# Kernel tuning notes

Hardware: AMD Instinct MI355X
Metric: run time of the kernel (lower is better)

The kernel has to match this reference:

```python
import jax, jax.numpy as jnp
import numpy as np

# channel indices (consistent with INPUT_CHANNELS=6)
WALL, SRC_REAL, SRC_IMAG, GATE_REAL, GATE_IMAG = 0, 1, 2, 3, 4
READOUT_THRESHOLD = 0.35
EPS = 1e-08


def _neighbor_sum(a):
    # zero-padded 4-neighbor shift-sum over last two dims of [B,1,H,W]
    H, W = a.shape[-2], a.shape[-1]
    p = jnp.pad(a, ((0, 0), (0, 0), (1, 1), (1, 1)))
    return (p[:, :, 0:H, 1:W + 1] + p[:, :, 2:H + 2, 1:W + 1]
            + p[:, :, 1:H + 1, 0:W] + p[:, :, 1:H + 1, 2:W + 2])


def _phase_vectors(phase_classes):
    k = jnp.arange(phase_classes, dtype=jnp.float32)
    th = 2.0 * jnp.pi * k / phase_classes
    return jnp.stack([jnp.cos(th), jnp.sin(th)], axis=1)  # [P,2]


def _fixed_logits(vec, phase_classes):
    phases = _phase_vectors(phase_classes)
    mag2 = jnp.sum(vec ** 2, axis=1)
    none = (READOUT_THRESHOLD * READOUT_THRESHOLD - mag2) * 8.0
    phase_logits = (vec @ phases.T - READOUT_THRESHOLD) * 12.0
    return jnp.concatenate([none[:, None], phase_logits], axis=1)


def setup_inputs() -> dict:
    key = jax.random.key(0)
    k1, k2 = jax.random.split(key)
    x = jax.random.uniform(k1, (32, 6, 256, 256), dtype=jnp.float32)
    target = jax.random.randint(k2, (32, 2), 0, 256, dtype=jnp.int64 if jax.config.jax_enable_x64 else jnp.int32)
    return {"x": x, "target": target, "steps": 24}


def reference(x, target, steps):
    phase_classes = 8
    free = 1.0 - x[:, WALL:WALL + 1]
    gate_r = x[:, GATE_REAL:GATE_REAL + 1]
    gate_i = x[:, GATE_IMAG:GATE_IMAG + 1]
    wallf = (x[:, WALL:WALL + 1] > 0.5).astype(x.dtype)

    real = x[:, SRC_REAL:SRC_REAL + 1] * free
    imag = x[:, SRC_IMAG:SRC_IMAG + 1] * free
    written = (real ** 2 + imag ** 2) > EPS
    state_r, state_i = real, imag

    def step(carry, _):
        real, imag, sr, si, written = carry
        inc_r = _neighbor_sum(real)
        inc_i = _neighbor_sum(imag)
        # FIXED_PRISMION: complex multiply with gate
        nr = inc_r * gate_r - inc_i * gate_i
        ni = inc_r * gate_i + inc_i * gate_r
        pre_wall = jnp.mean(jnp.sqrt(nr * nr + ni * ni) * wallf)
        real = nr * free
        imag = ni * free
        active = ((real ** 2 + imag ** 2) > EPS) & (~written)
        sr = jnp.where(active, real, sr)
        si = jnp.where(active, imag, si)
        written = written | active
        real = jnp.where(active, real, jnp.zeros_like(real))
        imag = jnp.where(active, imag, jnp.zeros_like(imag))
        act = jnp.mean(jnp.abs(real) + jnp.abs(imag))
        return (real, imag, sr, si, written), (pre_wall, act)

    (real, imag, state_r, state_i, written), (pre_walls, acts) = jax.lax.scan(
        step, (real, imag, state_r, state_i, written), None, length=int(steps))

    vec_map = jnp.concatenate([state_r, state_i], axis=1)  # [B,2,H,W]
    wall = x[:, WALL:WALL + 1] > 0.5
    leak = jnp.mean((((jnp.sum(vec_map ** 2, axis=1, keepdims=True) ** 0.5) > 0.5) & wall).astype(x.dtype))
    pre_wall_mean = jnp.mean(pre_walls)
    act_mean = jnp.mean(acts)

    b = jnp.arange(vec_map.shape[0])
    vec = vec_map[b, :, target[:, 0], target[:, 1]]  # [B,2]
    logits = _fixed_logits(vec, phase_classes)
    return logits, leak, pre_wall_mean, act_mean
```

## Files before the change

kernel.cpp:

```cpp
#include <hip/hip_runtime.h>
#include <stdint.h>

#define EPSV 1e-8f
#define HH 256
#define WW 256
#define NB 32
#define STEPS 24
#define PLANE (HH * WW)
#define NCELL (NB * PLANE)
#define NBLK 2048
#define TBLK 512
#define CAP 8192
#define FIXS 68719476736.0


__device__ __forceinline__ float block_fsum(float v, float* sm) {
  #pragma unroll
  for (int o = 32; o; o >>= 1) v += __shfl_down(v, o, 64);
  if ((threadIdx.x & 63) == 0) sm[threadIdx.x >> 6] = v;
  __syncthreads();
  float r = 0.0f;
  if (threadIdx.x == 0) r = ((sm[0] + sm[1]) + sm[2]) + sm[3];
  __syncthreads();
  return r;
}

__device__ __forceinline__ int block_isum(int v, int* sm) {
  #pragma unroll
  for (int o = 32; o; o >>= 1) v += __shfl_down(v, o, 64);
  if ((threadIdx.x & 63) == 0) sm[threadIdx.x >> 6] = v;
  __syncthreads();
  int r = 0;
  if (threadIdx.x == 0) r = sm[0] + sm[1] + sm[2] + sm[3];
  __syncthreads();
  return r;
}

__device__ __forceinline__ int block_any(int v, int* sm) {
  if (threadIdx.x == 0) sm[0] = 0;
  __syncthreads();
  if (v) sm[0] = 1;
  __syncthreads();
  int r = sm[0];
  __syncthreads();
  return r;
}

__global__ __launch_bounds__(128) void zero_kernel(int* __restrict__ ctrl) {
  ctrl[threadIdx.x] = 0;
}

__device__ __forceinline__ float2 init_rn(const float* __restrict__ xw, int y, int xc) {
  if ((unsigned)y >= (unsigned)HH || (unsigned)xc >= (unsigned)WW)
    return make_float2(0.f, 0.f);
  const int yx = y * WW + xc;
  const float fr = __fsub_rn(1.0f, xw[yx]);
  return make_float2(__fmul_rn(xw[PLANE + yx], fr), __fmul_rn(xw[2 * PLANE + yx], fr));
}

__device__ __forceinline__ float2 pre0_rn(const float* __restrict__ xw, int y, int xc) {
  float2 up = init_rn(xw, y - 1, xc);
  float2 dn = init_rn(xw, y + 1, xc);
  float2 lf = init_rn(xw, y, xc - 1);
  float2 rg = init_rn(xw, y, xc + 1);
  float inc_r = __fadd_rn(__fadd_rn(__fadd_rn(up.x, dn.x), lf.x), rg.x);
  float inc_i = __fadd_rn(__fadd_rn(__fadd_rn(up.y, dn.y), lf.y), rg.y);
  const int yx = y * WW + xc;
  const float gr = xw[3 * PLANE + yx], gi = xw[4 * PLANE + yx];
  return make_float2(__fsub_rn(__fmul_rn(inc_r, gr), __fmul_rn(inc_i, gi)),
                     __fadd_rn(__fmul_rn(inc_r, gi), __fmul_rn(inc_i, gr)));
}

__device__ __forceinline__ float2 val0_abm(const float* __restrict__ xw,
                                           const uint32_t* __restrict__ abm,
                                           int cbase, int y, int xc) {
  if ((unsigned)y >= (unsigned)HH || (unsigned)xc >= (unsigned)WW)
    return make_float2(0.f, 0.f);
  const int c = cbase + y * WW + xc;
  if (!((abm[c >> 5] >> (c & 31)) & 1u)) return make_float2(0.f, 0.f);
  float2 p = pre0_rn(xw, y, xc);
  const float fr = __fsub_rn(1.0f, xw[y * WW + xc]);
  return make_float2(__fmul_rn(p.x, fr), __fmul_rn(p.y, fr));
}

__global__ __launch_bounds__(256) void fused0_kernel(
    const float* __restrict__ x, const int* __restrict__ target,
    uint32_t* __restrict__ wrw, uint32_t* __restrict__ wrw1,
    uint32_t* __restrict__ abm,
    float* __restrict__ pw_part, float* __restrict__ act_part,
    int* __restrict__ ileak_part, float* __restrict__ vec,
    int* __restrict__ ctrl, int* __restrict__ list, uint32_t* __restrict__ cbm) {
  __shared__ float smf[4];
  __shared__ int smi[4];
  const int tx = threadIdx.x;
  const int blk = blockIdx.x;
  const int b = blk >> 6;
  const int y0 = (blk & 63) << 2;
  const int cbase = b * PLANE;
  const float* xw = x + (size_t)b * 6 * PLANE;
  const int t0 = target[b * 2], t1 = target[b * 2 + 1];

  if (tx < 32) { cbm[blk * 32 + tx] = 0; wrw1[blk * 32 + tx] = 0; }

  float pw = 0.0f, act = 0.0f;
  int leak = 0, any_act = 0;

  float2 rm = init_rn(xw, y0 - 1, tx);
  float2 rc = init_rn(xw, y0, tx);

  #pragma unroll
  for (int k = 0; k < 4; ++k) {
    const int y = y0 + k, yx = y * WW + tx;
    float2 rp = init_rn(xw, y + 1, tx);
    float2 lf = init_rn(xw, y, tx - 1);
    float2 rg = init_rn(xw, y, tx + 1);

    float inc_r = __fadd_rn(__fadd_rn(__fadd_rn(rm.x, rp.x), lf.x), rg.x);
    float inc_i = __fadd_rn(__fadd_rn(__fadd_rn(rm.y, rp.y), lf.y), rg.y);
    const float gr = xw[3 * PLANE + yx], gi = xw[4 * PLANE + yx];
    const float wall = xw[yx];

    float nr = __fsub_rn(__fmul_rn(inc_r, gr), __fmul_rn(inc_i, gi));
    float ni = __fadd_rn(__fmul_rn(inc_r, gi), __fmul_rn(inc_i, gr));
    if (wall > 0.5f) pw += sqrtf(nr * nr + ni * ni);

    const float fr = __fsub_rn(1.0f, wall);
    float r = __fmul_rn(nr, fr);
    float i = __fmul_rn(ni, fr);
    float mag0 = __fadd_rn(__fmul_rn(r, r), __fmul_rn(i, i));
    float magI = __fadd_rn(__fmul_rn(rc.x, rc.x), __fmul_rn(rc.y, rc.y));
    bool writtenI = magI > EPSV;
    bool active = (mag0 > EPSV) && !writtenI;

    if (magI > 0.25f && wall > 0.5f) ++leak;
    if (active && mag0 > 0.25f && wall > 0.5f) ++leak;

    if (active) { act += fabsf(r) + fabsf(i); any_act = 1; }

    if (y == t0 && tx == t1) {
      vec[2 * b] = active ? r : rc.x;
      vec[2 * b + 1] = active ? i : rc.y;
    }

    unsigned long long ba = __ballot(active);
    unsigned long long bw = __ballot(writtenI || active);
    if ((tx & 63) == 0) {
      const int w = (cbase + yx) >> 5;
      uint2 v; v.x = (uint32_t)bw; v.y = (uint32_t)(bw >> 32);
      *(uint2*)&wrw[w] = v;
      uint2 a; a.x = (uint32_t)ba; a.y = (uint32_t)(ba >> 32);
      *(uint2*)&abm[w] = a;
    }

    if (ba) {
      const int lane = tx & 63;
      const int ldr = __ffsll((unsigned long long)ba) - 1;
      unsigned lbase = 0;
      if (lane == ldr)
        lbase = atomicAdd((unsigned*)&ctrl[51], (unsigned)__popcll(ba));
      lbase = (unsigned)__shfl((int)lbase, ldr, 64);
      if (active) {
        unsigned pos = lbase + (unsigned)__popcll(ba & ((1ull << lane) - 1ull));
        if (pos < CAP) list[pos] = cbase + yx;
      }
    }
    rm = rc; rc = rp;
  }

  float pws = block_fsum(pw, smf);
  float acs = block_fsum(act, smf);
  int lks = block_isum(leak, smi);
  if (tx == 0) { pw_part[blk] = pws; act_part[blk] = acs; ileak_part[blk] = lks; }
  if (block_any(any_act, smi) && tx == 0) ctrl[1] = 1;
}

__global__ __launch_bounds__(512) void sparse1_kernel(
    const float* __restrict__ x, const int* __restrict__ target,
    float2* __restrict__ bufA, const uint32_t* __restrict__ wrw,
    uint32_t* __restrict__ wrw1, const uint32_t* __restrict__ abm,
    const int* __restrict__ list, uint32_t* __restrict__ cbm,
    int* __restrict__ ctrl, float* __restrict__ vec) {
  __shared__ long long smp[512];
  const int t = threadIdx.x;
  const int n0 = ctrl[51];
  if (n0 > CAP || n0 == 0) return;

  long long pwf = 0, actf = 0;
  int leak = 0;

  for (int idx = blockIdx.x * 512 + t; idx < 5 * n0; idx += gridDim.x * 512) {
    const int i = idx / 5, d = idx - 5 * i;
    int cell = list[i];
    int yx = cell & 0xFFFF;
    int y = yx >> 8, xx = yx & 255;
    if (d == 1) { if (y == 0) continue;       cell -= WW; y -= 1; }
    else if (d == 2) { if (y == HH - 1) continue;  cell += WW; y += 1; }
    else if (d == 3) { if (xx == 0) continue;      cell -= 1;  xx -= 1; }
    else if (d == 4) { if (xx == WW - 1) continue; cell += 1;  xx += 1; }
    const uint32_t bit = 1u << (cell & 31);
    if (atomicOr(&cbm[cell >> 5], bit) & bit) continue;

    const int bb = cell >> 16;
    const int cbase = bb * PLANE;
    yx = cell & 0xFFFF;
    const float* xw = x + (size_t)bb * 6 * PLANE;

    float2 up = val0_abm(xw, abm, cbase, y - 1, xx);
    float2 dn = val0_abm(xw, abm, cbase, y + 1, xx);
    float2 lf = val0_abm(xw, abm, cbase, y, xx - 1);
    float2 rg = val0_abm(xw, abm, cbase, y, xx + 1);
    float inc_r = __fadd_rn(__fadd_rn(__fadd_rn(up.x, dn.x), lf.x), rg.x);
    float inc_i = __fadd_rn(__fadd_rn(__fadd_rn(up.y, dn.y), lf.y), rg.y);
    float gr = xw[3 * PLANE + yx], gi = xw[4 * PLANE + yx];
    float wall = xw[yx];
    float nr = __fsub_rn(__fmul_rn(inc_r, gr), __fmul_rn(inc_i, gi));
    float ni = __fadd_rn(__fmul_rn(inc_r, gi), __fmul_rn(inc_i, gr));
    if (wall > 0.5f) pwf += (long long)((double)sqrtf(nr * nr + ni * ni) * FIXS);
    const float fr = __fsub_rn(1.0f, wall);
    float r = __fmul_rn(nr, fr);
    float i2 = __fmul_rn(ni, fr);
    float mag = __fadd_rn(__fmul_rn(r, r), __fmul_rn(i2, i2));
    bool wr = (wrw[cell >> 5] >> (cell & 31)) & 1u;
    bool active = (mag > EPSV) && !wr;
    float outr = active ? r : 0.0f;
    float outi = active ? i2 : 0.0f;
    bufA[cell] = make_float2(outr, outi);
    actf += (long long)((double)(fabsf(outr) + fabsf(outi)) * FIXS);
    if (active) {
      atomicOr(&wrw1[cell >> 5], bit);
      ctrl[2] = 1;
      if (mag > 0.25f && wall > 0.5f) ++leak;
      if (y == target[bb * 2] && xx == target[bb * 2 + 1]) {
        vec[2 * bb] = r; vec[2 * bb + 1] = i2;
      }
    }
  }

  smp[t] = pwf; __syncthreads();
  for (int o = 256; o; o >>= 1) { if (t < o) smp[t] += smp[t + o]; __syncthreads(); }
  if (t == 0 && smp[0]) atomicAdd((unsigned long long*)&ctrl[56], (unsigned long long)smp[0]);
  __syncthreads();
  smp[t] = actf; __syncthreads();
  for (int o = 256; o; o >>= 1) { if (t < o) smp[t] += smp[t + o]; __syncthreads(); }
  if (t == 0 && smp[0]) atomicAdd((unsigned long long*)&ctrl[58], (unsigned long long)smp[0]);
  __syncthreads();
  smp[t] = leak; __syncthreads();
  for (int o = 256; o; o >>= 1) { if (t < o) smp[t] += smp[t + o]; __syncthreads(); }
  if (t == 0 && smp[0]) atomicAdd(&ctrl[52], (int)smp[0]);
}

__device__ __forceinline__ void grid_barrier(int* bar) {
  __syncthreads();
  if (threadIdx.x == 0) {
    __threadfence();
    __hip_atomic_fetch_add(bar, 1, __ATOMIC_RELEASE, __HIP_MEMORY_SCOPE_AGENT);
    int guard = 0;
    while (__hip_atomic_load(bar, __ATOMIC_ACQUIRE, __HIP_MEMORY_SCOPE_AGENT) < TBLK) {
      if (++guard > (1 << 22)) break;
    }
  }
  __syncthreads();
}

__global__ __launch_bounds__(256, 2) void tailfinal_kernel(
    const float* __restrict__ x, const int* __restrict__ target,
    float2* __restrict__ bufA, float2* __restrict__ bufB,
    const uint32_t* __restrict__ wrw, const uint32_t* __restrict__ wrw1,
    const uint32_t* __restrict__ abm, const uint32_t* __restrict__ cbm,
    float* __restrict__ pw_part, float* __restrict__ act_part,
    int* __restrict__ ileak_part, float* __restrict__ vec,
    int* __restrict__ ctrl, float* __restrict__ out) {
  __shared__ double smd[256];
  __shared__ float smf[4];
  __shared__ int smi[4];
  const int tx = threadIdx.x;
  const int blk = blockIdx.x;
  int* cnt = ctrl;
  int* bar = ctrl + 25;
  const int n0 = ctrl[51];
  const bool ov = (n0 > CAP);
  const int sstart = ov ? 1 : 2;

  if (cnt[sstart] != 0) {
    const int b = blk >> 4;
    const int y0 = (blk & 15) << 4;
    const int cbase = b * PLANE;
    const float* xw  = x + (size_t)b * 6 * PLANE;
    const float* xgr = xw + 3 * PLANE;
    const float* xgi = xw + 4 * PLANE;
    const int t0 = target[b * 2], t1 = target[b * 2 + 1];

    float wallr[16];
    unsigned wrmask = 0;
    #pragma unroll
    for (int k = 0; k < 16; ++k) {
      const int c = cbase + (y0 + k) * WW + tx;
      wallr[k] = xw[(y0 + k) * WW + tx];
      if (((wrw[c >> 5] | wrw1[c >> 5]) >> (c & 31)) & 1u) wrmask |= (1u << k);
    }

    if (ov) {
      #pragma unroll
      for (int k = 0; k < 16; ++k)
        bufB[cbase + (y0 + k) * WW + tx] = val0_abm(xw, abm, cbase, y0 + k, tx);
    } else {
      #pragma unroll
      for (int k = 0; k < 16; ++k) {
        const int c = cbase + (y0 + k) * WW + tx;
        if (!((cbm[c >> 5] >> (c & 31)) & 1u)) bufA[c] = make_float2(0.f, 0.f);
      }
    }
    grid_barrier(&bar[24]);

    const float2* cur0 = ov ? (const float2*)bufB : (const float2*)bufA;
    float2* nxt0 = ov ? bufA : bufB;

    for (int s = sstart; s < STEPS; ++s) {
      if (__hip_atomic_load(&cnt[s], __ATOMIC_RELAXED, __HIP_MEMORY_SCOPE_AGENT) == 0) break;
      const int p = (s - sstart) & 1;
      const float2* __restrict__ cur = p ? (const float2*)nxt0 : cur0;
      float2* __restrict__ nxt = p ? (float2*)cur0 : nxt0;

      float pw = 0.0f, act = 0.0f;
      int leak_s = 0, any_act = 0;

      float2 rowm = (y0 > 0) ? cur[cbase + (y0 - 1) * WW + tx] : make_float2(0.f, 0.f);
      float2 rowc = cur[cbase + y0 * WW + tx];

      #pragma unroll
      for (int k = 0; k < 16; ++k) {
        const int y = y0 + k, yx = y * WW + tx;
        float2 rowp = (y < HH - 1) ? cur[cbase + yx + WW] : make_float2(0.f, 0.f);
        float2 lft  = (tx > 0)      ? cur[cbase + yx - 1] : make_float2(0.f, 0.f);
        float2 rgt  = (tx < WW - 1) ? cur[cbase + yx + 1] : make_float2(0.f, 0.f);

        float inc_r = __fadd_rn(__fadd_rn(__fadd_rn(rowm.x, rowp.x), lft.x), rgt.x);
        float inc_i = __fadd_rn(__fadd_rn(__fadd_rn(rowm.y, rowp.y), lft.y), rgt.y);
        float gr = xgr[yx], gi = xgi[yx];
        float wall = wallr[k];

        float nr = __fsub_rn(__fmul_rn(inc_r, gr), __fmul_rn(inc_i, gi));
        float ni = __fadd_rn(__fmul_rn(inc_r, gi), __fmul_rn(inc_i, gr));
        if (wall > 0.5f) pw += sqrtf(nr * nr + ni * ni);

        const float fr = __fsub_rn(1.0f, wall);
        float r = __fmul_rn(nr, fr);
        float i = __fmul_rn(ni, fr);
        float mag = __fadd_rn(__fmul_rn(r, r), __fmul_rn(i, i));
        bool active = (mag > EPSV) && !((wrmask >> k) & 1u);

        float outr = active ? r : 0.0f;
        float outi = active ? i : 0.0f;
        nxt[cbase + yx] = make_float2(outr, outi);
        act += fabsf(outr) + fabsf(outi);

        if (active) {
          wrmask |= (1u << k);
          any_act = 1;
          if (mag > 0.25f && wall > 0.5f) ++leak_s;
          if (y == t0 && tx == t1) { vec[2 * b] = r; vec[2 * b + 1] = i; }
        }
        rowm = rowc; rowc = rowp;
      }

      float pws = block_fsum(pw, smf);
      float acs = block_fsum(act, smf);
      int lks = block_isum(leak_s, smi);
      if (tx == 0) {
        pw_part[s * NBLK + blk] = pws;
        act_part[s * NBLK + blk] = acs;
        ileak_part[s * NBLK + blk] = lks;
      }
      if (block_any(any_act, smi) && tx == 0)
        __hip_atomic_store(&cnt[s + 1], 1, __ATOMIC_RELAXED, __HIP_MEMORY_SCOPE_AGENT);
      grid_barrier(&bar[s]);
    }
  }

  if (blk != 0) return;

  double pw = 0.0, ac = 0.0, lk = 0.0;
  for (int j = tx; j < NBLK; j += 256) {
    pw += (double)pw_part[j];
    ac += (double)act_part[j];
    lk += (double)ileak_part[j];
  }
  for (int s = sstart; s < STEPS; ++s) {
    if (cnt[s] == 0) break;
    for (int j = tx; j < TBLK; j += 256) {
      pw += (double)pw_part[s * NBLK + j];
      ac += (double)act_part[s * NBLK + j];
      lk += (double)ileak_part[s * NBLK + j];
    }
  }
  smd[tx] = pw; __syncthreads();
  for (int o = 128; o; o >>= 1) { if (tx < o) smd[tx] += smd[tx + o]; __syncthreads(); }
  double pws = smd[0]; __syncthreads();
  smd[tx] = ac; __syncthreads();
  for (int o = 128; o; o >>= 1) { if (tx < o) smd[tx] += smd[tx + o]; __syncthreads(); }
  double acs = smd[0]; __syncthreads();
  smd[tx] = lk; __syncthreads();
  for (int o = 128; o; o >>= 1) { if (tx < o) smd[tx] += smd[tx + o]; __syncthreads(); }
  double lks = smd[0];

  if (tx < NB) {
    float vr = vec[tx * 2], vi = vec[tx * 2 + 1];
    float mag2 = __fadd_rn(__fmul_rn(vr, vr), __fmul_rn(vi, vi));
    out[tx * 9] = (0.35f * 0.35f - mag2) * 8.0f;
    #pragma unroll
    for (int k = 0; k < 8; ++k) {
      float th = (float)(6.283185307179586 * (double)k) / 8.0f;
      float pl = (vr * cosf(th) + vi * sinf(th) - 0.35f) * 12.0f;
      out[tx * 9 + 1 + k] = pl;
    }
  }
  if (tx == 0) {
    pws += (double)((const long long*)ctrl)[28] / FIXS;
    acs += (double)((const long long*)ctrl)[29] / FIXS;
    lks += (double)ctrl[52];
    out[288] = (float)(lks / (double)NCELL);
    out[289] = (float)(pws / ((double)STEPS * (double)NCELL));
    out[290] = (float)(acs / ((double)STEPS * (double)NCELL));
  }
}

extern "C" void kernel_launch(void* const* d_in, const int* in_sizes, int n_in,
                              void* d_out, int out_size, void* d_ws, size_t ws_size,
                              hipStream_t stream) {
  const float* x = (const float*)d_in[0];
  const int* target = (const int*)d_in[1];

  char* ws = (char*)d_ws;
  float2* bufA = (float2*)ws;
  float2* bufB = bufA + NCELL;
  float* pw_part  = (float*)(bufB + NCELL);
  float* act_part = pw_part + STEPS * NBLK;
  int* ileak_part = (int*)(act_part + STEPS * NBLK);
  float* vec      = (float*)(ileak_part + STEPS * NBLK);
  uint32_t* wrw   = (uint32_t*)(vec + 2 * NB);
  uint32_t* wrw1  = wrw + NCELL / 32;
  uint32_t* abm   = wrw1 + NCELL / 32;
  uint32_t* cbm   = abm + NCELL / 32;
  int* list       = (int*)(cbm + NCELL / 32);
  int* ctrl       = list + CAP;

  zero_kernel<<<1, 128, 0, stream>>>(ctrl);
  fused0_kernel<<<NBLK, 256, 0, stream>>>(x, target, wrw, wrw1, abm,
                                          pw_part, act_part, ileak_part, vec,
                                          ctrl, list, cbm);
  sparse1_kernel<<<16, 512, 0, stream>>>(x, target, bufA, wrw, wrw1, abm,
                                         list, cbm, ctrl, vec);
  tailfinal_kernel<<<TBLK, 256, 0, stream>>>(x, target, bufA, bufB, wrw, wrw1,
                                             abm, cbm, pw_part, act_part,
                                             ileak_part, vec, ctrl, (float*)d_out);
}
```

Measured before the change: 43.16 us.

## Fold sparse step-1 kernel into tail kernel and use wave shuffles for stencil

The sparse second-step kernel is merged into the persistent tail kernel as a first phase, followed by a grid barrier. This removes one kernel launch and lets all 512 blocks share the sparse work instead of 16. In the dense first kernel, left and right neighbours now come from wave shuffles instead of global reloads, and the wall value is carried across rows. In exchange it adds an extra grid barrier, reuses barrier counter slots, and adds per-active-cell threadfences.

```diff
diff --git a/kernel.cpp b/kernel.cpp
--- a/kernel.cpp
+++ b/kernel.cpp
@@ -106,25 +106,39 @@
   int leak = 0, any_act = 0;
 
   float2 rm = init_rn(xw, y0 - 1, tx);
-  float2 rc = init_rn(xw, y0, tx);
+  float wallc = xw[y0 * WW + tx];
+  float2 rc;
+  {
+    const float fr = __fsub_rn(1.0f, wallc);
+    rc = make_float2(__fmul_rn(xw[PLANE + y0 * WW + tx], fr),
+                     __fmul_rn(xw[2 * PLANE + y0 * WW + tx], fr));
+  }
 
   #pragma unroll
   for (int k = 0; k < 4; ++k) {
     const int y = y0 + k, yx = y * WW + tx;
-    float2 rp = init_rn(xw, y + 1, tx);
-    float2 lf = init_rn(xw, y, tx - 1);
-    float2 rg = init_rn(xw, y, tx + 1);
+    float wallp = 0.0f;
+    float2 rp = make_float2(0.f, 0.f);
+    if (y + 1 < HH) {
+      wallp = xw[yx + WW];
+      const float fr = __fsub_rn(1.0f, wallp);
+      rp = make_float2(__fmul_rn(xw[PLANE + yx + WW], fr),
+                       __fmul_rn(xw[2 * PLANE + yx + WW], fr));
+    }
+    float2 lf = make_float2(__shfl_up(rc.x, 1, 64), __shfl_up(rc.y, 1, 64));
+    float2 rg = make_float2(__shfl_down(rc.x, 1, 64), __shfl_down(rc.y, 1, 64));
+    if ((tx & 63) == 0)  lf = init_rn(xw, y, tx - 1);
+    if ((tx & 63) == 63) rg = init_rn(xw, y, tx + 1);
 
     float inc_r = __fadd_rn(__fadd_rn(__fadd_rn(rm.x, rp.x), lf.x), rg.x);
     float inc_i = __fadd_rn(__fadd_rn(__fadd_rn(rm.y, rp.y), lf.y), rg.y);
     const float gr = xw[3 * PLANE + yx], gi = xw[4 * PLANE + yx];
-    const float wall = xw[yx];
 
     float nr = __fsub_rn(__fmul_rn(inc_r, gr), __fmul_rn(inc_i, gi));
     float ni = __fadd_rn(__fmul_rn(inc_r, gi), __fmul_rn(inc_i, gr));
-    if (wall > 0.5f) pw += sqrtf(nr * nr + ni * ni);
-
-    const float fr = __fsub_rn(1.0f, wall);
+    if (wallc > 0.5f) pw += sqrtf(nr * nr + ni * ni);
+
+    const float fr = __fsub_rn(1.0f, wallc);
     float r = __fmul_rn(nr, fr);
     float i = __fmul_rn(ni, fr);
     float mag0 = __fadd_rn(__fmul_rn(r, r), __fmul_rn(i, i));
@@ -132,8 +146,8 @@
     bool writtenI = magI > EPSV;
     bool active = (mag0 > EPSV) && !writtenI;
 
-    if (magI > 0.25f && wall > 0.5f) ++leak;
-    if (active && mag0 > 0.25f && wall > 0.5f) ++leak;
+    if (magI > 0.25f && wallc > 0.5f) ++leak;
+    if (active && mag0 > 0.25f && wallc > 0.5f) ++leak;
 
     if (active) { act += fabsf(r) + fabsf(i); any_act = 1; }
 
@@ -164,7 +178,7 @@
         if (pos < CAP) list[pos] = cbase + yx;
       }
     }
-    rm = rc; rc = rp;
+    rm = rc; rc = rp; wallc = wallp;
   }
 
   float pws = block_fsum(pw, smf);
@@ -172,81 +186,6 @@
   int lks = block_isum(leak, smi);
   if (tx == 0) { pw_part[blk] = pws; act_part[blk] = acs; ileak_part[blk] = lks; }
   if (block_any(any_act, smi) && tx == 0) ctrl[1] = 1;
-}
-
-__global__ __launch_bounds__(512) void sparse1_kernel(
-    const float* __restrict__ x, const int* __restrict__ target,
-    float2* __restrict__ bufA, const uint32_t* __restrict__ wrw,
-    uint32_t* __restrict__ wrw1, const uint32_t* __restrict__ abm,
-    const int* __restrict__ list, uint32_t* __restrict__ cbm,
-    int* __restrict__ ctrl, float* __restrict__ vec) {
-  __shared__ long long smp[512];
-  const int t = threadIdx.x;
-  const int n0 = ctrl[51];
-  if (n0 > CAP || n0 == 0) return;
-
-  long long pwf = 0, actf = 0;
-  int leak = 0;
-
-  for (int idx = blockIdx.x * 512 + t; idx < 5 * n0; idx += gridDim.x * 512) {
-    const int i = idx / 5, d = idx - 5 * i;
-    int cell = list[i];
-    int yx = cell & 0xFFFF;
-    int y = yx >> 8, xx = yx & 255;
-    if (d == 1) { if (y == 0) continue;       cell -= WW; y -= 1; }
-    else if (d == 2) { if (y == HH - 1) continue;  cell += WW; y += 1; }
-    else if (d == 3) { if (xx == 0) continue;      cell -= 1;  xx -= 1; }
-    else if (d == 4) { if (xx == WW - 1) continue; cell += 1;  xx += 1; }
-    const uint32_t bit = 1u << (cell & 31);
-    if (atomicOr(&cbm[cell >> 5], bit) & bit) continue;
-
-    const int bb = cell >> 16;
-    const int cbase = bb * PLANE;
-    yx = cell & 0xFFFF;
-    const float* xw = x + (size_t)bb * 6 * PLANE;
-
-    float2 up = val0_abm(xw, abm, cbase, y - 1, xx);
-    float2 dn = val0_abm(xw, abm, cbase, y + 1, xx);
-    float2 lf = val0_abm(xw, abm, cbase, y, xx - 1);
-    float2 rg = val0_abm(xw, abm, cbase, y, xx + 1);
-    float inc_r = __fadd_rn(__fadd_rn(__fadd_rn(up.x, dn.x), lf.x), rg.x);
-    float inc_i = __fadd_rn(__fadd_rn(__fadd_rn(up.y, dn.y), lf.y), rg.y);
-    float gr = xw[3 * PLANE + yx], gi = xw[4 * PLANE + yx];
-    float wall = xw[yx];
-    float nr = __fsub_rn(__fmul_rn(inc_r, gr), __fmul_rn(inc_i, gi));
-    float ni = __fadd_rn(__fmul_rn(inc_r, gi), __fmul_rn(inc_i, gr));
-    if (wall > 0.5f) pwf += (long long)((double)sqrtf(nr * nr + ni * ni) * FIXS);
-    const float fr = __fsub_rn(1.0f, wall);
-    float r = __fmul_rn(nr, fr);
-    float i2 = __fmul_rn(ni, fr);
-    float mag = __fadd_rn(__fmul_rn(r, r), __fmul_rn(i2, i2));
-    bool wr = (wrw[cell >> 5] >> (cell & 31)) & 1u;
-    bool active = (mag > EPSV) && !wr;
-    float outr = active ? r : 0.0f;
-    float outi = active ? i2 : 0.0f;
-    bufA[cell] = make_float2(outr, outi);
-    actf += (long long)((double)(fabsf(outr) + fabsf(outi)) * FIXS);
-    if (active) {
-      atomicOr(&wrw1[cell >> 5], bit);
-      ctrl[2] = 1;
-      if (mag > 0.25f && wall > 0.5f) ++leak;
-      if (y == target[bb * 2] && xx == target[bb * 2 + 1]) {
-        vec[2 * bb] = r; vec[2 * bb + 1] = i2;
-      }
-    }
-  }
-
-  smp[t] = pwf; __syncthreads();
-  for (int o = 256; o; o >>= 1) { if (t < o) smp[t] += smp[t + o]; __syncthreads(); }
-  if (t == 0 && smp[0]) atomicAdd((unsigned long long*)&ctrl[56], (unsigned long long)smp[0]);
-  __syncthreads();
-  smp[t] = actf; __syncthreads();
-  for (int o = 256; o; o >>= 1) { if (t < o) smp[t] += smp[t + o]; __syncthreads(); }
-  if (t == 0 && smp[0]) atomicAdd((unsigned long long*)&ctrl[58], (unsigned long long)smp[0]);
-  __syncthreads();
-  smp[t] = leak; __syncthreads();
-  for (int o = 256; o; o >>= 1) { if (t < o) smp[t] += smp[t + o]; __syncthreads(); }
-  if (t == 0 && smp[0]) atomicAdd(&ctrl[52], (int)smp[0]);
 }
 
 __device__ __forceinline__ void grid_barrier(int* bar) {
@@ -262,14 +201,16 @@
   __syncthreads();
 }
 
-__global__ __launch_bounds__(256, 2) void tailfinal_kernel(
+__global__ __launch_bounds__(256, 2) void megatail_kernel(
     const float* __restrict__ x, const int* __restrict__ target,
     float2* __restrict__ bufA, float2* __restrict__ bufB,
-    const uint32_t* __restrict__ wrw, const uint32_t* __restrict__ wrw1,
-    const uint32_t* __restrict__ abm, const uint32_t* __restrict__ cbm,
+    const uint32_t* __restrict__ wrw, uint32_t* __restrict__ wrw1,
+    const uint32_t* __restrict__ abm, uint32_t* __restrict__ cbm,
+    const int* __restrict__ list,
     float* __restrict__ pw_part, float* __restrict__ act_part,
     int* __restrict__ ileak_part, float* __restrict__ vec,
     int* __restrict__ ctrl, float* __restrict__ out) {
+  __shared__ long long smp[256];
   __shared__ double smd[256];
   __shared__ float smf[4];
   __shared__ int smi[4];
@@ -281,6 +222,72 @@
   const bool ov = (n0 > CAP);
   const int sstart = ov ? 1 : 2;
 
+  long long pwf = 0, actf = 0;
+  int leak = 0;
+  if (!ov && n0 > 0) {
+    for (int idx = blk * 256 + tx; idx < 5 * n0; idx += TBLK * 256) {
+      const int i = idx / 5, d = idx - 5 * i;
+      int cell = list[i];
+      int yx = cell & 0xFFFF;
+      int y = yx >> 8, xx = yx & 255;
+      if (d == 1) { if (y == 0) continue;       cell -= WW; y -= 1; }
+      else if (d == 2) { if (y == HH - 1) continue;  cell += WW; y += 1; }
+      else if (d == 3) { if (xx == 0) continue;      cell -= 1;  xx -= 1; }
+      else if (d == 4) { if (xx == WW - 1) continue; cell += 1;  xx += 1; }
+      const uint32_t bit = 1u << (cell & 31);
+      if (atomicOr(&cbm[cell >> 5], bit) & bit) continue;
+
+      const int bb = cell >> 16;
+      const int cbase = bb * PLANE;
+      yx = cell & 0xFFFF;
+      const float* xw = x + (size_t)bb * 6 * PLANE;
+
+      float2 up = val0_abm(xw, abm, cbase, y - 1, xx);
+      float2 dn = val0_abm(xw, abm, cbase, y + 1, xx);
+      float2 lf = val0_abm(xw, abm, cbase, y, xx - 1);
+      float2 rg = val0_abm(xw, abm, cbase, y, xx + 1);
+      float inc_r = __fadd_rn(__fadd_rn(__fadd_rn(up.x, dn.x), lf.x), rg.x);
+      float inc_i = __fadd_rn(__fadd_rn(__fadd_rn(up.y, dn.y), lf.y), rg.y);
+      float gr = xw[3 * PLANE + yx], gi = xw[4 * PLANE + yx];
+      float wall = xw[yx];
+      float nr = __fsub_rn(__fmul_rn(inc_r, gr), __fmul_rn(inc_i, gi));
+      float ni = __fadd_rn(__fmul_rn(inc_r, gi), __fmul_rn(inc_i, gr));
+      if (wall > 0.5f) pwf += (long long)((double)sqrtf(nr * nr + ni * ni) * FIXS);
+      const float fr = __fsub_rn(1.0f, wall);
+      float r = __fmul_rn(nr, fr);
+      float i2 = __fmul_rn(ni, fr);
+      float mag = __fadd_rn(__fmul_rn(r, r), __fmul_rn(i2, i2));
+      bool wr = (wrw[cell >> 5] >> (cell & 31)) & 1u;
+      bool active = (mag > EPSV) && !wr;
+      float outr = active ? r : 0.0f;
+      float outi = active ? i2 : 0.0f;
+      bufA[cell] = make_float2(outr, outi);
+      actf += (long long)((double)(fabsf(outr) + fabsf(outi)) * FIXS);
+      if (active) {
+        atomicOr(&wrw1[cell >> 5], bit);
+        __hip_atomic_store(&cnt[2], 1, __ATOMIC_RELAXED, __HIP_MEMORY_SCOPE_AGENT);
+        if (mag > 0.25f && wall > 0.5f) ++leak;
+        if (y == target[bb * 2] && xx == target[bb * 2 + 1]) {
+          vec[2 * bb] = r; vec[2 * bb + 1] = i2;
+        }
+        __threadfence();
+      }
+    }
+  }
+  smp[tx] = pwf; __syncthreads();
+  for (int o = 128; o; o >>= 1) { if (tx < o) smp[tx] += smp[tx + o]; __syncthreads(); }
+  if (tx == 0 && smp[0]) atomicAdd((unsigned long long*)&ctrl[56], (unsigned long long)smp[0]);
+  __syncthreads();
+  smp[tx] = actf; __syncthreads();
+  for (int o = 128; o; o >>= 1) { if (tx < o) smp[tx] += smp[tx + o]; __syncthreads(); }
+  if (tx == 0 && smp[0]) atomicAdd((unsigned long long*)&ctrl[58], (unsigned long long)smp[0]);
+  __syncthreads();
+  smp[tx] = leak; __syncthreads();
+  for (int o = 128; o; o >>= 1) { if (tx < o) smp[tx] += smp[tx + o]; __syncthreads(); }
+  if (tx == 0 && smp[0]) atomicAdd(&ctrl[52], (int)smp[0]);
+
+  grid_barrier(&bar[24]);
+
   if (cnt[sstart] != 0) {
     const int b = blk >> 4;
     const int y0 = (blk & 15) << 4;
@@ -310,7 +317,7 @@
         if (!((cbm[c >> 5] >> (c & 31)) & 1u)) bufA[c] = make_float2(0.f, 0.f);
       }
     }
-    grid_barrier(&bar[24]);
+    grid_barrier(&bar[0]);
 
     const float2* cur0 = ov ? (const float2*)bufB : (const float2*)bufA;
     float2* nxt0 = ov ? bufA : bufB;
@@ -448,9 +455,7 @@
   fused0_kernel<<<NBLK, 256, 0, stream>>>(x, target, wrw, wrw1, abm,
                                           pw_part, act_part, ileak_part, vec,
                                           ctrl, list, cbm);
-  sparse1_kernel<<<16, 512, 0, stream>>>(x, target, bufA, wrw, wrw1, abm,
-                                         list, cbm, ctrl, vec);
-  tailfinal_kernel<<<TBLK, 256, 0, stream>>>(x, target, bufA, bufB, wrw, wrw1,
-                                             abm, cbm, pw_part, act_part,
-                                             ileak_part, vec, ctrl, (float*)d_out);
-}
+  megatail_kernel<<<TBLK, 256, 0, stream>>>(x, target, bufA, bufB, wrw, wrw1,
+                                            abm, cbm, list, pw_part, act_part,
+                                            ileak_part, vec, ctrl, (float*)d_out);
+}
```

Measured after the change: 114.9 us. +166.3%, slower.

## Finalize outputs in sparse kernel when propagation dies, skip tail; shuffle neighbors

Applied to the files above, without the earlier changes.

The first-step kernel now takes left and right neighbor values from adjacent lanes with wave shuffles, and reuses the wall value carried from the previous row. This removes redundant global loads of the source and wall planes. The sparse second-step kernel gains a last-block-done counter. When no cell became active, that last block reduces the partial sums and writes the final logits and means, and the tail kernel returns early. This avoids the 512-block tail launch doing barrier work when propagation has already stopped, at the cost of an atomic counter and an extra serial reduction in one block.

```diff
diff --git a/kernel.cpp b/kernel.cpp
--- a/kernel.cpp
+++ b/kernel.cpp
@@ -10,6 +10,7 @@
 #define NCELL (NB * PLANE)
 #define NBLK 2048
 #define TBLK 512
+#define SBLK 16
 #define CAP 8192
 #define FIXS 68719476736.0
 
@@ -106,25 +107,39 @@
   int leak = 0, any_act = 0;
 
   float2 rm = init_rn(xw, y0 - 1, tx);
-  float2 rc = init_rn(xw, y0, tx);
+  float wallc = xw[y0 * WW + tx];
+  float2 rc;
+  {
+    const float fr = __fsub_rn(1.0f, wallc);
+    rc = make_float2(__fmul_rn(xw[PLANE + y0 * WW + tx], fr),
+                     __fmul_rn(xw[2 * PLANE + y0 * WW + tx], fr));
+  }
 
   #pragma unroll
   for (int k = 0; k < 4; ++k) {
     const int y = y0 + k, yx = y * WW + tx;
-    float2 rp = init_rn(xw, y + 1, tx);
-    float2 lf = init_rn(xw, y, tx - 1);
-    float2 rg = init_rn(xw, y, tx + 1);
+    float wallp = 0.0f;
+    float2 rp = make_float2(0.f, 0.f);
+    if (y + 1 < HH) {
+      wallp = xw[yx + WW];
+      const float fr = __fsub_rn(1.0f, wallp);
+      rp = make_float2(__fmul_rn(xw[PLANE + yx + WW], fr),
+                       __fmul_rn(xw[2 * PLANE + yx + WW], fr));
+    }
+    float2 lf = make_float2(__shfl_up(rc.x, 1, 64), __shfl_up(rc.y, 1, 64));
+    float2 rg = make_float2(__shfl_down(rc.x, 1, 64), __shfl_down(rc.y, 1, 64));
+    if ((tx & 63) == 0)  lf = init_rn(xw, y, tx - 1);
+    if ((tx & 63) == 63) rg = init_rn(xw, y, tx + 1);
 
     float inc_r = __fadd_rn(__fadd_rn(__fadd_rn(rm.x, rp.x), lf.x), rg.x);
     float inc_i = __fadd_rn(__fadd_rn(__fadd_rn(rm.y, rp.y), lf.y), rg.y);
     const float gr = xw[3 * PLANE + yx], gi = xw[4 * PLANE + yx];
-    const float wall = xw[yx];
 
     float nr = __fsub_rn(__fmul_rn(inc_r, gr), __fmul_rn(inc_i, gi));
     float ni = __fadd_rn(__fmul_rn(inc_r, gi), __fmul_rn(inc_i, gr));
-    if (wall > 0.5f) pw += sqrtf(nr * nr + ni * ni);
-
-    const float fr = __fsub_rn(1.0f, wall);
+    if (wallc > 0.5f) pw += sqrtf(nr * nr + ni * ni);
+
+    const float fr = __fsub_rn(1.0f, wallc);
     float r = __fmul_rn(nr, fr);
     float i = __fmul_rn(ni, fr);
     float mag0 = __fadd_rn(__fmul_rn(r, r), __fmul_rn(i, i));
@@ -132,8 +147,8 @@
     bool writtenI = magI > EPSV;
     bool active = (mag0 > EPSV) && !writtenI;
 
-    if (magI > 0.25f && wall > 0.5f) ++leak;
-    if (active && mag0 > 0.25f && wall > 0.5f) ++leak;
+    if (magI > 0.25f && wallc > 0.5f) ++leak;
+    if (active && mag0 > 0.25f && wallc > 0.5f) ++leak;
 
     if (active) { act += fabsf(r) + fabsf(i); any_act = 1; }
 
@@ -164,7 +179,7 @@
         if (pos < CAP) list[pos] = cbase + yx;
       }
     }
-    rm = rc; rc = rp;
+    rm = rc; rc = rp; wallc = wallp;
   }
 
   float pws = block_fsum(pw, smf);
@@ -179,16 +194,20 @@
     float2* __restrict__ bufA, const uint32_t* __restrict__ wrw,
     uint32_t* __restrict__ wrw1, const uint32_t* __restrict__ abm,
     const int* __restrict__ list, uint32_t* __restrict__ cbm,
-    int* __restrict__ ctrl, float* __restrict__ vec) {
+    int* __restrict__ ctrl, float* __restrict__ vec,
+    const float* __restrict__ pw_part, const float* __restrict__ act_part,
+    const int* __restrict__ ileak_part, float* __restrict__ out) {
   __shared__ long long smp[512];
+  __shared__ double smd[512];
+  __shared__ int swin;
   const int t = threadIdx.x;
   const int n0 = ctrl[51];
-  if (n0 > CAP || n0 == 0) return;
+  if (n0 > CAP) return;
 
   long long pwf = 0, actf = 0;
   int leak = 0;
 
-  for (int idx = blockIdx.x * 512 + t; idx < 5 * n0; idx += gridDim.x * 512) {
+  for (int idx = blockIdx.x * 512 + t; idx < 5 * n0; idx += SBLK * 512) {
     const int i = idx / 5, d = idx - 5 * i;
     int cell = list[i];
     int yx = cell & 0xFFFF;
@@ -228,7 +247,7 @@
     actf += (long long)((double)(fabsf(outr) + fabsf(outi)) * FIXS);
     if (active) {
       atomicOr(&wrw1[cell >> 5], bit);
-      ctrl[2] = 1;
+      __hip_atomic_store(&ctrl[2], 1, __ATOMIC_RELAXED, __HIP_MEMORY_SCOPE_AGENT);
       if (mag > 0.25f && wall > 0.5f) ++leak;
       if (y == target[bb * 2] && xx == target[bb * 2 + 1]) {
         vec[2 * bb] = r; vec[2 * bb + 1] = i2;
@@ -247,6 +266,54 @@
   smp[t] = leak; __syncthreads();
   for (int o = 256; o; o >>= 1) { if (t < o) smp[t] += smp[t + o]; __syncthreads(); }
   if (t == 0 && smp[0]) atomicAdd(&ctrl[52], (int)smp[0]);
+
+  __syncthreads();
+  if (t == 0) {
+    __threadfence();
+    int old = __hip_atomic_fetch_add(&ctrl[60], 1, __ATOMIC_ACQ_REL,
+                                     __HIP_MEMORY_SCOPE_AGENT);
+    swin = (old == SBLK - 1) ? 1 : 0;
+  }
+  __syncthreads();
+  if (!swin) return;
+  if (__hip_atomic_load(&ctrl[2], __ATOMIC_RELAXED, __HIP_MEMORY_SCOPE_AGENT) != 0)
+    return;
+
+  double pw = 0.0, ac = 0.0, lk = 0.0;
+  for (int j = t; j < NBLK; j += 512) {
+    pw += (double)pw_part[j];
+    ac += (double)act_part[j];
+    lk += (double)ileak_part[j];
+  }
+  smd[t] = pw; __syncthreads();
+  for (int o = 256; o; o >>= 1) { if (t < o) smd[t] += smd[t + o]; __syncthreads(); }
+  double pws = smd[0]; __syncthreads();
+  smd[t] = ac; __syncthreads();
+  for (int o = 256; o; o >>= 1) { if (t < o) smd[t] += smd[t + o]; __syncthreads(); }
+  double acs = smd[0]; __syncthreads();
+  smd[t] = lk; __syncthreads();
+  for (int o = 256; o; o >>= 1) { if (t < o) smd[t] += smd[t + o]; __syncthreads(); }
+  double lks = smd[0];
+
+  if (t < NB) {
+    float vr = vec[t * 2], vi = vec[t * 2 + 1];
+    float mag2 = __fadd_rn(__fmul_rn(vr, vr), __fmul_rn(vi, vi));
+    out[t * 9] = (0.35f * 0.35f - mag2) * 8.0f;
+    #pragma unroll
+    for (int k = 0; k < 8; ++k) {
+      float th = (float)(6.283185307179586 * (double)k) / 8.0f;
+      float pl = (vr * cosf(th) + vi * sinf(th) - 0.35f) * 12.0f;
+      out[t * 9 + 1 + k] = pl;
+    }
+  }
+  if (t == 0) {
+    pws += (double)((const long long*)ctrl)[28] / FIXS;
+    acs += (double)((const long long*)ctrl)[29] / FIXS;
+    lks += (double)ctrl[52];
+    out[288] = (float)(lks / (double)NCELL);
+    out[289] = (float)(pws / ((double)STEPS * (double)NCELL));
+    out[290] = (float)(acs / ((double)STEPS * (double)NCELL));
+  }
 }
 
 __device__ __forceinline__ void grid_barrier(int* bar) {
@@ -280,6 +347,7 @@
   const int n0 = ctrl[51];
   const bool ov = (n0 > CAP);
   const int sstart = ov ? 1 : 2;
+  if (!ov && cnt[2] == 0) return;
 
   if (cnt[sstart] != 0) {
     const int b = blk >> 4;
@@ -448,8 +516,10 @@
   fused0_kernel<<<NBLK, 256, 0, stream>>>(x, target, wrw, wrw1, abm,
                                           pw_part, act_part, ileak_part, vec,
                                           ctrl, list, cbm);
-  sparse1_kernel<<<16, 512, 0, stream>>>(x, target, bufA, wrw, wrw1, abm,
-                                         list, cbm, ctrl, vec);
+  sparse1_kernel<<<SBLK, 512, 0, stream>>>(x, target, bufA, wrw, wrw1, abm,
+                                           list, cbm, ctrl, vec,
+                                           pw_part, act_part, ileak_part,
+                                           (float*)d_out);
   tailfinal_kernel<<<TBLK, 256, 0, stream>>>(x, target, bufA, bufB, wrw, wrw1,
                                              abm, cbm, pw_part, act_part,
                                              ileak_part, vec, ctrl, (float*)d_out);
```

After: 42.31 us. 2.0% less time.
